# Kernel optimization log

Hardware: AMD Instinct MI355X
Metric: run time of the kernel (lower is better)

The kernel has to match this reference:

```python
import math
import jax, jax.numpy as jnp
import numpy as np

_TEMP_CLAMP = 4.6

def _l2n(x):
    # torch F.normalize: x / max(||x||, eps)
    return x / jnp.maximum(jnp.linalg.norm(x, axis=-1, keepdims=True), 1e-12)

def setup_inputs() -> dict:
    key = jax.random.key(0)
    k1, k2, k3, k4, k5 = jax.random.split(key, 5)
    B, S, D, V, NNEG = 1024, 64, 128, 100000, 2048
    hidden = jax.random.normal(k1, (B, S, D), dtype=jnp.float32)
    y = jax.random.randint(k2, (B, S), 0, V, dtype=jnp.int64)
    embed_table = jax.random.normal(k3, (V, D), dtype=jnp.float32)
    sampling_probs = jax.random.uniform(k4, (V,), dtype=jnp.float32, minval=1e-6, maxval=1.0)
    sampled_indices = jax.random.randint(k5, (NNEG,), 0, V, dtype=jnp.int64)
    log_temperature = jnp.asarray(math.log(1.0 / 0.07), dtype=jnp.float32)
    return {"hidden": hidden, "y": y, "embed_table": embed_table,
            "sampling_probs": sampling_probs, "sampled_indices": sampled_indices,
            "log_temperature": log_temperature}

def reference(hidden, y, embed_table, sampling_probs, sampled_indices, log_temperature):
    D = hidden.shape[-1]
    h = hidden.reshape(-1, D)          # [N, D]
    yf = y.reshape(-1)                 # [N]
    valid = (yf != 0)                  # padding mask (static-shape weighting instead of boolean gather)

    true_p = sampling_probs[yf]                # [N]
    samp_p = sampling_probs[sampled_indices]   # [NNEG]
    e_pos = embed_table[yf]                    # [N, D]
    e_neg = embed_table[sampled_indices]       # [NNEG, D]

    temp = jnp.exp(jnp.minimum(log_temperature, _TEMP_CLAMP))
    hn = _l2n(h)
    pos_logits = jnp.sum(hn * _l2n(e_pos), axis=-1) * temp        # [N]
    neg_logits = (hn @ _l2n(e_neg).T) * temp                      # [N, NNEG]

    collision = yf[:, None] == sampled_indices[None, :]
    neg_logits = jnp.where(collision, -1e9, neg_logits)

    pos_adj = pos_logits - jnp.log(true_p + 1e-10)                # [N]
    neg_adj = neg_logits - jnp.log(samp_p + 1e-10)[None, :]       # [N, NNEG]
    logits = jnp.concatenate([pos_adj[:, None], neg_adj], axis=1) # [N, 1+NNEG]

    per_row = -jax.nn.log_softmax(logits, axis=-1)[:, 0]          # CE with label 0
    w = valid.astype(per_row.dtype)
    return jnp.sum(per_row * w) / jnp.maximum(jnp.sum(w), 1.0)
```

## Files before the change

kernel.cpp:

```cpp
#include <hip/hip_runtime.h>
#include <math.h>

#define TPB 256
#define NNEG 2048
#define D 128
#define CHUNK 64
#define NCH (NNEG / CHUNK)
#define L2E 1.44269504088896340736f

typedef __attribute__((ext_vector_type(8))) short bf16x8;
typedef __attribute__((ext_vector_type(4))) float f32x4;

#define MFMA16 __builtin_amdgcn_mfma_f32_16x16x32_bf16

static __device__ __forceinline__ unsigned int f2bf(float f) {
    unsigned int u = __float_as_uint(f);
    return (u + 0x7FFFu + ((u >> 16) & 1u)) >> 16;
}

static __device__ __forceinline__ void stage16(const void* g, void* l) {
    __builtin_amdgcn_global_load_lds(
        (const __attribute__((address_space(1))) unsigned int*)g,
        (__attribute__((address_space(3))) unsigned int*)l, 16, 0, 0);
}

__global__ __launch_bounds__(TPB) void sspe_prep(
    const float* __restrict__ embed,
    const float* __restrict__ sprobs,
    const int* __restrict__ sidx,
    unsigned int* __restrict__ en_bf,
    float* __restrict__ ln_samp)
{
    const int t = threadIdx.x;
    const int wave = t >> 6;
    const int lane = t & 63;
    const int j = blockIdx.x * 4 + wave;
    const int idx = sidx[j];

    float2 v = reinterpret_cast<const float2*>(embed)[(size_t)idx * 64 + lane];
    float ss = v.x * v.x + v.y * v.y;
    ss += __shfl_xor(ss, 1);
    ss += __shfl_xor(ss, 2);
    ss += __shfl_xor(ss, 4);
    ss += __shfl_xor(ss, 8);
    ss += __shfl_xor(ss, 16);
    ss += __shfl_xor(ss, 32);
    const float rinv = 1.0f / fmaxf(sqrtf(ss), 1e-12f);
    en_bf[(size_t)j * 64 + lane] = f2bf(v.x * rinv) | (f2bf(v.y * rinv) << 16);
    if (lane == 0) ln_samp[j] = logf(sprobs[idx] + 1e-10f);
}

__global__ __launch_bounds__(TPB, 4) void sspe_main(
    const float* __restrict__ hidden,
    const int* __restrict__ y,
    const float* __restrict__ embed,
    const float* __restrict__ sprobs,
    const int* __restrict__ sidx,
    const float* __restrict__ ltemp,
    const unsigned int* __restrict__ en_bf,
    const float* __restrict__ ln_samp,
    float2* __restrict__ partials)
{
    const int t = threadIdx.x;
    const int wave = t >> 6;
    const int lane = t & 63;
    const int rb = blockIdx.x * 64;

    __shared__ __align__(16) unsigned char smem[2 * CHUNK * 256];
    __shared__ float pos_s[64];
    __shared__ int   ys[64];
    __shared__ float sums[64];

    const float temp = __builtin_amdgcn_exp2f(fminf(ltemp[0], 4.6f) * L2E);
    const float t2 = temp * L2E;
    const float Mln = temp + 14.0f;
    const float M2 = Mln * L2E;

    if (t < 64) ys[t] = y[rb + t];
    __syncthreads();

    #pragma unroll 1
    for (int i = 0; i < 16; i += 4) {
        float2 h2[4], e2[4];
        int yi[4];
        #pragma unroll
        for (int u = 0; u < 4; ++u) {
            const int lr = wave * 16 + i + u;
            h2[u] = reinterpret_cast<const float2*>(hidden)[(size_t)(rb + lr) * 64 + lane];
            yi[u] = ys[lr];
        }
        #pragma unroll
        for (int u = 0; u < 4; ++u)
            e2[u] = reinterpret_cast<const float2*>(embed)[(size_t)yi[u] * 64 + lane];
        float ss[4], es[4], dt[4];
        #pragma unroll
        for (int u = 0; u < 4; ++u) {
            ss[u] = h2[u].x * h2[u].x + h2[u].y * h2[u].y;
            es[u] = e2[u].x * e2[u].x + e2[u].y * e2[u].y;
            dt[u] = h2[u].x * e2[u].x + h2[u].y * e2[u].y;
        }
        #pragma unroll
        for (int m = 1; m <= 32; m <<= 1)
            #pragma unroll
            for (int u = 0; u < 4; ++u) {
                ss[u] += __shfl_xor(ss[u], m);
                es[u] += __shfl_xor(es[u], m);
                dt[u] += __shfl_xor(dt[u], m);
            }
        #pragma unroll
        for (int u = 0; u < 4; ++u) {
            const int lr = wave * 16 + i + u;
            const float rinv = 1.0f / fmaxf(sqrtf(ss[u]), 1e-12f);
            const unsigned int uu = f2bf(h2[u].x * rinv) | (f2bf(h2[u].y * rinv) << 16);
            const int rx = (lr & 7) << 4;
            *reinterpret_cast<unsigned int*>(smem + lr * 256 + ((lane * 4) ^ rx)) = uu;
            if (lane == 0)
                pos_s[lr] = dt[u] * rinv * (1.0f / fmaxf(sqrtf(es[u]), 1e-12f)) * temp
                            - logf(sprobs[yi[u]] + 1e-10f);
        }
    }
    __syncthreads();

    bf16x8 A[4];
    {
        const int row = wave * 16 + (lane & 15);
        const int rx = (lane & 7) << 4;
        const unsigned char* rp = smem + row * 256;
        #pragma unroll
        for (int ks = 0; ks < 4; ++ks)
            A[ks] = *reinterpret_cast<const bf16x8*>(
                rp + ((ks * 64 + ((lane >> 4) << 4)) ^ rx));
    }
    __syncthreads();

    const int cj = lane & 15;
    const int rgrp = lane >> 4;
    int yv[4];
    float l[4];
    #pragma unroll
    for (int j = 0; j < 4; ++j) {
        yv[j] = ys[wave * 16 + rgrp * 4 + j];
        l[j] = 0.0f;
    }

    unsigned int soff[4];
    #pragma unroll
    for (int i = 0; i < 4; ++i) {
        const unsigned int doff = i * 4096 + wave * 1024 + lane * 16;
        soff[i] = doff ^ (((doff >> 8) & 7) << 4);
    }
    const unsigned char* en = reinterpret_cast<const unsigned char*>(en_bf);
    const int rx = (cj & 7) << 4;

    #pragma unroll
    for (int i = 0; i < 4; ++i)
        stage16(en + soff[i], smem + i * 4096 + wave * 1024);

    #pragma unroll 1
    for (int ch = 0; ch < NCH; ++ch) {
        const int cur = (ch & 1) << 14;
        const int nxt = cur ^ 16384;
        __syncthreads();

        float lk[4];
        int ci[4];
        #pragma unroll
        for (int tt = 0; tt < 4; ++tt) {
            lk[tt] = ln_samp[ch * 64 + tt * 16 + cj];
            ci[tt] = sidx[ch * 64 + tt * 16 + cj];
        }

        if (ch + 1 < NCH) {
            const unsigned char* enn = en + (size_t)(ch + 1) * 16384;
            #pragma unroll
            for (int i = 0; i < 4; ++i)
                stage16(enn + soff[i], smem + nxt + i * 4096 + wave * 1024);
        }

        f32x4 c[4];
        #pragma unroll
        for (int tt = 0; tt < 4; ++tt) {
            const unsigned char* bp = smem + cur + (tt * 16 + cj) * 256;
            c[tt] = (f32x4){0.f, 0.f, 0.f, 0.f};
            #pragma unroll
            for (int ks = 0; ks < 4; ++ks) {
                const bf16x8 b = *reinterpret_cast<const bf16x8*>(
                    bp + ((ks * 64 + (rgrp << 4)) ^ rx));
                c[tt] = MFMA16(A[ks], b, c[tt], 0, 0, 0);
            }
        }

        #pragma unroll
        for (int tt = 0; tt < 4; ++tt) {
            const float nl2 = fmaf(lk[tt], -L2E, -M2);
            #pragma unroll
            for (int j = 0; j < 4; ++j) {
                const float a = fmaf(c[tt][j], t2, nl2);
                const float e = __builtin_amdgcn_exp2f(a);
                l[j] += (ci[tt] == yv[j]) ? 0.0f : e;
            }
        }
    }

    #pragma unroll
    for (int j = 0; j < 4; ++j) {
        float v = l[j];
        v += __shfl_xor(v, 1);
        v += __shfl_xor(v, 2);
        v += __shfl_xor(v, 4);
        v += __shfl_xor(v, 8);
        l[j] = v;
    }
    if (cj == 0) {
        #pragma unroll
        for (int j = 0; j < 4; ++j)
            sums[wave * 16 + rgrp * 4 + j] = l[j];
    }
    __syncthreads();

    if (t < 64) {
        const float s = sums[t];
        const float pa = pos_s[t];
        const float stot = s + __builtin_amdgcn_exp2f(fmaf(pa, L2E, -M2));
        float per = Mln + logf(stot) - pa;
        float w = (ys[t] != 0) ? 1.0f : 0.0f;
        per *= w;
        #pragma unroll
        for (int msk = 1; msk < 64; msk <<= 1) {
            per += __shfl_xor(per, msk);
            w += __shfl_xor(w, msk);
        }
        if (t == 0) partials[blockIdx.x] = make_float2(per, w);
    }
}

__global__ __launch_bounds__(TPB) void sspe_finalize(
    const float2* __restrict__ partials, int n, float* __restrict__ out)
{
    __shared__ float ssum[TPB];
    __shared__ float scnt[TPB];
    const int t = threadIdx.x;
    float s = 0.0f, c = 0.0f;
    for (int i = t; i < n; i += TPB) {
        const float2 p = partials[i];
        s += p.x; c += p.y;
    }
    ssum[t] = s; scnt[t] = c;
    __syncthreads();
    for (int k = TPB / 2; k > 0; k >>= 1) {
        if (t < k) { ssum[t] += ssum[t + k]; scnt[t] += scnt[t + k]; }
        __syncthreads();
    }
    if (t == 0) out[0] = ssum[0] / fmaxf(scnt[0], 1.0f);
}

extern "C" void kernel_launch(void* const* d_in, const int* in_sizes, int n_in,
                              void* d_out, int out_size, void* d_ws, size_t ws_size,
                              hipStream_t stream) {
    const float* hidden = (const float*)d_in[0];
    const int*   yv     = (const int*)d_in[1];
    const float* embed  = (const float*)d_in[2];
    const float* sprobs = (const float*)d_in[3];
    const int*   sidx   = (const int*)d_in[4];
    const float* ltemp  = (const float*)d_in[5];
    float* out = (float*)d_out;

    const int nrows = in_sizes[1];
    const int nblocks = nrows / 64;

    char* w = (char*)d_ws;
    unsigned int* en_bf  = (unsigned int*)w;
    float*  ln_samp      = (float*)(w + (size_t)NNEG * D * 2);
    float2* partials     = (float2*)(w + (size_t)NNEG * D * 2 + NNEG * 4);

    sspe_prep<<<NNEG / 4, TPB, 0, stream>>>(embed, sprobs, sidx, en_bf, ln_samp);
    sspe_main<<<nblocks, TPB, 0, stream>>>(hidden, yv, embed, sprobs, sidx, ltemp,
                                           en_bf, ln_samp, partials);
    sspe_finalize<<<1, TPB, 0, stream>>>(partials, nblocks, out);
}
```

Before: 80.53 us.

## Process 128 rows per block so each staged negative tile feeds two MFMA row tiles

Each block now handles 128 rows, 32 per wave, with two A fragments per wave. Every B fragment loaded from LDS is reused for two MFMAs, which halves the negative-embedding staging and LDS reads per row. The LDS layout of the staged chunk is changed to a fragment-contiguous order so each lane reads a linear 16-byte slot with no XOR swizzle. The cost is more registers (launch bounds drop to 2 blocks) and half as many blocks, which lowers occupancy and grid parallelism.

```diff
diff --git a/kernel.cpp b/kernel.cpp
--- a/kernel.cpp
+++ b/kernel.cpp
@@ -6,6 +6,8 @@
 #define D 128
 #define CHUNK 64
 #define NCH (NNEG / CHUNK)
+#define RPB 128
+#define RPW 32
 #define L2E 1.44269504088896340736f
 
 typedef __attribute__((ext_vector_type(8))) short bf16x8;
@@ -50,7 +52,7 @@
     if (lane == 0) ln_samp[j] = logf(sprobs[idx] + 1e-10f);
 }
 
-__global__ __launch_bounds__(TPB, 4) void sspe_main(
+__global__ __launch_bounds__(TPB, 2) void sspe_main(
     const float* __restrict__ hidden,
     const int* __restrict__ y,
     const float* __restrict__ embed,
@@ -64,28 +66,29 @@
     const int t = threadIdx.x;
     const int wave = t >> 6;
     const int lane = t & 63;
-    const int rb = blockIdx.x * 64;
-
-    __shared__ __align__(16) unsigned char smem[2 * CHUNK * 256];
-    __shared__ float pos_s[64];
-    __shared__ int   ys[64];
-    __shared__ float sums[64];
+    const int rb = blockIdx.x * RPB;
+
+    __shared__ __align__(16) unsigned char smem[RPB * 256];
+    __shared__ float pos_s[RPB];
+    __shared__ int   ys[RPB];
+    __shared__ float sums[RPB];
+    __shared__ float2 red2[4];
 
     const float temp = __builtin_amdgcn_exp2f(fminf(ltemp[0], 4.6f) * L2E);
     const float t2 = temp * L2E;
     const float Mln = temp + 14.0f;
     const float M2 = Mln * L2E;
 
-    if (t < 64) ys[t] = y[rb + t];
+    if (t < RPB) ys[t] = y[rb + t];
     __syncthreads();
 
     #pragma unroll 1
-    for (int i = 0; i < 16; i += 4) {
+    for (int i = 0; i < RPW; i += 4) {
         float2 h2[4], e2[4];
         int yi[4];
         #pragma unroll
         for (int u = 0; u < 4; ++u) {
-            const int lr = wave * 16 + i + u;
+            const int lr = wave * RPW + i + u;
             h2[u] = reinterpret_cast<const float2*>(hidden)[(size_t)(rb + lr) * 64 + lane];
             yi[u] = ys[lr];
         }
@@ -109,7 +112,7 @@
             }
         #pragma unroll
         for (int u = 0; u < 4; ++u) {
-            const int lr = wave * 16 + i + u;
+            const int lr = wave * RPW + i + u;
             const float rinv = 1.0f / fmaxf(sqrtf(ss[u]), 1e-12f);
             const unsigned int uu = f2bf(h2[u].x * rinv) | (f2bf(h2[u].y * rinv) << 16);
             const int rx = (lr & 7) << 4;
@@ -121,116 +124,131 @@
     }
     __syncthreads();
 
-    bf16x8 A[4];
+    bf16x8 A0[4], A1[4];
     {
-        const int row = wave * 16 + (lane & 15);
+        const int row0 = wave * RPW + (lane & 15);
         const int rx = (lane & 7) << 4;
-        const unsigned char* rp = smem + row * 256;
-        #pragma unroll
-        for (int ks = 0; ks < 4; ++ks)
-            A[ks] = *reinterpret_cast<const bf16x8*>(
-                rp + ((ks * 64 + ((lane >> 4) << 4)) ^ rx));
+        #pragma unroll
+        for (int ks = 0; ks < 4; ++ks) {
+            const int col = (ks * 64 + ((lane >> 4) << 4)) ^ rx;
+            A0[ks] = *reinterpret_cast<const bf16x8*>(smem + row0 * 256 + col);
+            A1[ks] = *reinterpret_cast<const bf16x8*>(smem + (row0 + 16) * 256 + col);
+        }
     }
     __syncthreads();
 
     const int cj = lane & 15;
     const int rgrp = lane >> 4;
-    int yv[4];
-    float l[4];
+    int yv0[4], yv1[4];
+    float l0[4], l1[4];
     #pragma unroll
     for (int j = 0; j < 4; ++j) {
-        yv[j] = ys[wave * 16 + rgrp * 4 + j];
-        l[j] = 0.0f;
+        yv0[j] = ys[wave * RPW + rgrp * 4 + j];
+        yv1[j] = ys[wave * RPW + 16 + rgrp * 4 + j];
+        l0[j] = 0.0f;
+        l1[j] = 0.0f;
     }
 
     unsigned int soff[4];
     #pragma unroll
     for (int i = 0; i < 4; ++i) {
-        const unsigned int doff = i * 4096 + wave * 1024 + lane * 16;
-        soff[i] = doff ^ (((doff >> 8) & 7) << 4);
+        const int d = wave * 4 + i;
+        soff[i] = (unsigned int)((d >> 2) * 4096 + (lane & 15) * 256
+                                 + (d & 3) * 64 + (lane >> 4) * 16);
     }
     const unsigned char* en = reinterpret_cast<const unsigned char*>(en_bf);
-    const int rx = (cj & 7) << 4;
 
     #pragma unroll
     for (int i = 0; i < 4; ++i)
-        stage16(en + soff[i], smem + i * 4096 + wave * 1024);
+        stage16(en + soff[i], smem + (wave * 4 + i) * 1024);
 
     #pragma unroll 1
     for (int ch = 0; ch < NCH; ++ch) {
         const int cur = (ch & 1) << 14;
-        const int nxt = cur ^ 16384;
         __syncthreads();
 
         float lk[4];
         int ci[4];
         #pragma unroll
-        for (int tt = 0; tt < 4; ++tt) {
-            lk[tt] = ln_samp[ch * 64 + tt * 16 + cj];
-            ci[tt] = sidx[ch * 64 + tt * 16 + cj];
+        for (int nt = 0; nt < 4; ++nt) {
+            lk[nt] = ln_samp[ch * 64 + nt * 16 + cj];
+            ci[nt] = sidx[ch * 64 + nt * 16 + cj];
         }
 
         if (ch + 1 < NCH) {
             const unsigned char* enn = en + (size_t)(ch + 1) * 16384;
             #pragma unroll
             for (int i = 0; i < 4; ++i)
-                stage16(enn + soff[i], smem + nxt + i * 4096 + wave * 1024);
-        }
-
-        f32x4 c[4];
-        #pragma unroll
-        for (int tt = 0; tt < 4; ++tt) {
-            const unsigned char* bp = smem + cur + (tt * 16 + cj) * 256;
-            c[tt] = (f32x4){0.f, 0.f, 0.f, 0.f};
+                stage16(enn + soff[i], smem + (cur ^ 16384) + (wave * 4 + i) * 1024);
+        }
+
+        const unsigned char* bb = smem + cur + lane * 16;
+        f32x4 c0[4], c1[4];
+        #pragma unroll
+        for (int nt = 0; nt < 4; ++nt) {
+            c0[nt] = (f32x4){0.f, 0.f, 0.f, 0.f};
+            c1[nt] = (f32x4){0.f, 0.f, 0.f, 0.f};
             #pragma unroll
             for (int ks = 0; ks < 4; ++ks) {
-                const bf16x8 b = *reinterpret_cast<const bf16x8*>(
-                    bp + ((ks * 64 + (rgrp << 4)) ^ rx));
-                c[tt] = MFMA16(A[ks], b, c[tt], 0, 0, 0);
+                const bf16x8 b = *reinterpret_cast<const bf16x8*>(bb + (nt * 4 + ks) * 1024);
+                c0[nt] = MFMA16(A0[ks], b, c0[nt], 0, 0, 0);
+                c1[nt] = MFMA16(A1[ks], b, c1[nt], 0, 0, 0);
             }
         }
 
         #pragma unroll
-        for (int tt = 0; tt < 4; ++tt) {
-            const float nl2 = fmaf(lk[tt], -L2E, -M2);
+        for (int nt = 0; nt < 4; ++nt) {
+            const float nl2 = fmaf(lk[nt], -L2E, -M2);
             #pragma unroll
             for (int j = 0; j < 4; ++j) {
-                const float a = fmaf(c[tt][j], t2, nl2);
-                const float e = __builtin_amdgcn_exp2f(a);
-                l[j] += (ci[tt] == yv[j]) ? 0.0f : e;
+                const float a0 = fmaf(c0[nt][j], t2, nl2);
+                const float a1 = fmaf(c1[nt][j], t2, nl2);
+                const float e0 = __builtin_amdgcn_exp2f(a0);
+                const float e1 = __builtin_amdgcn_exp2f(a1);
+                l0[j] += (ci[nt] == yv0[j]) ? 0.0f : e0;
+                l1[j] += (ci[nt] == yv1[j]) ? 0.0f : e1;
             }
         }
     }
 
     #pragma unroll
     for (int j = 0; j < 4; ++j) {
-        float v = l[j];
-        v += __shfl_xor(v, 1);
-        v += __shfl_xor(v, 2);
-        v += __shfl_xor(v, 4);
-        v += __shfl_xor(v, 8);
-        l[j] = v;
+        float v0 = l0[j], v1 = l1[j];
+        v0 += __shfl_xor(v0, 1);  v1 += __shfl_xor(v1, 1);
+        v0 += __shfl_xor(v0, 2);  v1 += __shfl_xor(v1, 2);
+        v0 += __shfl_xor(v0, 4);  v1 += __shfl_xor(v1, 4);
+        v0 += __shfl_xor(v0, 8);  v1 += __shfl_xor(v1, 8);
+        l0[j] = v0;
+        l1[j] = v1;
     }
     if (cj == 0) {
         #pragma unroll
-        for (int j = 0; j < 4; ++j)
-            sums[wave * 16 + rgrp * 4 + j] = l[j];
-    }
-    __syncthreads();
-
-    if (t < 64) {
+        for (int j = 0; j < 4; ++j) {
+            sums[wave * RPW + rgrp * 4 + j] = l0[j];
+            sums[wave * RPW + 16 + rgrp * 4 + j] = l1[j];
+        }
+    }
+    __syncthreads();
+
+    float per = 0.0f, w = 0.0f;
+    if (t < RPB) {
         const float s = sums[t];
         const float pa = pos_s[t];
         const float stot = s + __builtin_amdgcn_exp2f(fmaf(pa, L2E, -M2));
-        float per = Mln + logf(stot) - pa;
-        float w = (ys[t] != 0) ? 1.0f : 0.0f;
-        per *= w;
-        #pragma unroll
-        for (int msk = 1; msk < 64; msk <<= 1) {
-            per += __shfl_xor(per, msk);
-            w += __shfl_xor(w, msk);
-        }
-        if (t == 0) partials[blockIdx.x] = make_float2(per, w);
+        w = (ys[t] != 0) ? 1.0f : 0.0f;
+        per = (Mln + logf(stot) - pa) * w;
+    }
+    #pragma unroll
+    for (int msk = 1; msk < 64; msk <<= 1) {
+        per += __shfl_xor(per, msk);
+        w += __shfl_xor(w, msk);
+    }
+    if (lane == 0) red2[wave] = make_float2(per, w);
+    __syncthreads();
+    if (t == 0) {
+        const float2 a = red2[0], b = red2[1], c = red2[2], d = red2[3];
+        partials[blockIdx.x] = make_float2(a.x + b.x + c.x + d.x,
+                                           a.y + b.y + c.y + d.y);
     }
 }
 
@@ -266,7 +284,7 @@
     float* out = (float*)d_out;
 
     const int nrows = in_sizes[1];
-    const int nblocks = nrows / 64;
+    const int nblocks = nrows / RPB;
 
     char* w = (char*)d_ws;
     unsigned int* en_bf  = (unsigned int*)w;
```

Result: slower. 95.82 us (+19.0%).
